# Kernel optimization log

Hardware: AMD Instinct MI355X
Metric: run time of the kernel (lower is better)

Reference implementation:

```python
import jax, jax.numpy as jnp
import numpy as np

D_K = 64  # key/query head dim used for the 1/sqrt(d_k) scale


def setup_inputs() -> dict:
    key0 = jax.random.key(0)
    kk, kq, kv = jax.random.split(key0, 3)
    B, H, S, DK, DV = 2, 16, 2048, 64, 64
    return {
        "key": jax.random.normal(kk, (B, H, S, DK), dtype=jnp.float32),
        "query": jax.random.normal(kq, (B, H, S, DK), dtype=jnp.float32),
        "value": jax.random.normal(kv, (B, H, S, DV), dtype=jnp.float32),
    }


def reference(key, query, value):
    # scaled dot-product attention per head: [B,H,S,S]
    scores = jnp.einsum("bhqd,bhkd->bhqk", query, key) / jnp.sqrt(jnp.asarray(D_K, query.dtype))
    attn = jax.nn.softmax(scores, axis=-1)
    out = jnp.einsum("bhqk,bhkv->bhqv", attn, value)  # [B,H,S,d_v]
    B, H, S, DV = out.shape
    # faithful to the torch .view: raw reshape (no head transpose)
    return out.reshape(B, S, H * DV)
```

## Files before the change

### kernel.cpp

```cpp
#include <hip/hip_runtime.h>

#define S_LEN 2048
#define DHEAD 64
#define BHEADS 32
#define NTILES 32
#define HEAD_ELEMS (S_LEN * DHEAD)
#define TENS_ELEMS (BHEADS * HEAD_ELEMS)
#define TILE_HALVES 4096

typedef _Float16 half8_t __attribute__((ext_vector_type(8)));
typedef _Float16 half4_t __attribute__((ext_vector_type(4)));
typedef _Float16 half2_t __attribute__((ext_vector_type(2)));
typedef float float4_t __attribute__((ext_vector_type(4)));

#define SC_LOG2E 0.18033688011112042f


__global__ __launch_bounds__(256) void prep_kernel(const float* __restrict__ K,
                                                   const float* __restrict__ V,
                                                   _Float16* __restrict__ Kf,
                                                   _Float16* __restrict__ Vf) {
    __shared__ _Float16 tile[64][72];
    const int bh = blockIdx.x >> 5;
    const int t = blockIdx.x & 31;
    const int tid = threadIdx.x;

    const float* Ksrc = K + (bh * S_LEN + t * 64) * DHEAD;
    const float4* vs = (const float4*)(V + (bh * S_LEN + t * 64) * DHEAD);
#pragma unroll
    for (int it = 0; it < 4; ++it) {
        int i = it * 256 + tid;
        float4 vv = vs[i];
        int r = i >> 4, c4 = (i & 15) * 4;
        half4_t hv = {(_Float16)vv.x, (_Float16)vv.y, (_Float16)vv.z, (_Float16)vv.w};
        *(half4_t*)&tile[r][c4] = hv;
    }

    _Float16* kd = Kf + (bh * NTILES + t) * TILE_HALVES;
#pragma unroll
    for (int it = 0; it < 2; ++it) {
        int c = it * 256 + tid;
        int f = c >> 6, lane = c & 63;
        int row = (f >> 1) * 16 + (lane & 15);
        int d0 = (f & 1) * 32 + (lane >> 4) * 8;
        const float4* s = (const float4*)(Ksrc + row * DHEAD + d0);
        float4 a = s[0], b = s[1];
        half8_t h = {(_Float16)(a.x * SC_LOG2E), (_Float16)(a.y * SC_LOG2E),
                     (_Float16)(a.z * SC_LOG2E), (_Float16)(a.w * SC_LOG2E),
                     (_Float16)(b.x * SC_LOG2E), (_Float16)(b.y * SC_LOG2E),
                     (_Float16)(b.z * SC_LOG2E), (_Float16)(b.w * SC_LOG2E)};
        *(half8_t*)(kd + c * 8) = h;
    }
    __syncthreads();

    _Float16* vd = Vf + (bh * NTILES + t) * TILE_HALVES;
#pragma unroll
    for (int it = 0; it < 2; ++it) {
        int c = it * 256 + tid;
        int fv = c >> 6, lane = c & 63;
        int vt = fv >> 1, ktp = fv & 1;
        int v = vt * 16 + (lane & 15);
        int g = lane >> 4;
        half8_t h;
#pragma unroll
        for (int j = 0; j < 8; ++j) {
            int key = ktp * 32 + (j >> 2) * 16 + g * 4 + (j & 3);
            h[j] = tile[key][v];
        }
        *(half8_t*)(vd + c * 8) = h;
    }
}


__global__ __launch_bounds__(256, 4) void attn_kernel(
    const float* __restrict__ Qf,
    const _Float16* __restrict__ Kf,
    const _Float16* __restrict__ Vf,
    float* __restrict__ out) {
    __shared__ float red[2][34][64];

    const int tid = threadIdx.x;
    const int wid = tid >> 6;
    const int lane = tid & 63;
    const int ln15 = lane & 15;
    const int g = lane >> 4;

    const int bh = blockIdx.x & 31;
    const int qidx = blockIdx.x >> 5;
    const int qsub = wid >> 1;
    const int ks = wid & 1;
    const int q0 = qidx * 64 + qsub * 32;
    const int t0 = ks * 16;

    const float* Qg = Qf + (bh * S_LEN + q0) * DHEAD;
    half8_t qf[2][2];
#pragma unroll
    for (int nq = 0; nq < 2; ++nq)
#pragma unroll
        for (int kh = 0; kh < 2; ++kh) {
            const float4* qs = (const float4*)(Qg + (nq * 16 + ln15) * DHEAD + kh * 32 + g * 8);
            float4 a = qs[0], b = qs[1];
            qf[nq][kh] = (half8_t){(_Float16)a.x, (_Float16)a.y, (_Float16)a.z, (_Float16)a.w,
                                   (_Float16)b.x, (_Float16)b.y, (_Float16)b.z, (_Float16)b.w};
        }

    const _Float16* kb = Kf + bh * (NTILES * TILE_HALVES) + t0 * TILE_HALVES;
    const _Float16* vb = Vf + bh * (NTILES * TILE_HALVES) + t0 * TILE_HALVES;
    const int lo = lane * 8;

    float lsum[2] = {0.f, 0.f};
    float4_t o[2][4];
#pragma unroll
    for (int nq = 0; nq < 2; ++nq)
#pragma unroll
        for (int vt = 0; vt < 4; ++vt) o[nq][vt] = (float4_t){0.f, 0.f, 0.f, 0.f};

#pragma unroll 2
    for (int t = 0; t < 16; ++t) {
        const int base = t * TILE_HALVES;

#pragma unroll
        for (int c = 0; c < 2; ++c) {
            half8_t kA[4], vA[4];
#pragma unroll
            for (int i = 0; i < 4; ++i)
                kA[i] = *(const half8_t*)(kb + base + (4 * c + i) * 512 + lo);
#pragma unroll
            for (int vt = 0; vt < 4; ++vt)
                vA[vt] = *(const half8_t*)(vb + base + (vt * 2 + c) * 512 + lo);

            half8_t pb[2];
#pragma unroll
            for (int h = 0; h < 2; ++h) {
                half8_t a0 = kA[h * 2];
                half8_t a1 = kA[h * 2 + 1];
#pragma unroll
                for (int nq = 0; nq < 2; ++nq) {
                    float4_t c0 = (float4_t){0.f, 0.f, 0.f, 0.f};
                    c0 = __builtin_amdgcn_mfma_f32_16x16x32_f16(a0, qf[nq][0], c0, 0, 0, 0);
                    c0 = __builtin_amdgcn_mfma_f32_16x16x32_f16(a1, qf[nq][1], c0, 0, 0, 0);
                    float p0 = __builtin_amdgcn_exp2f(c0[0]);
                    float p1 = __builtin_amdgcn_exp2f(c0[1]);
                    float p2 = __builtin_amdgcn_exp2f(c0[2]);
                    float p3 = __builtin_amdgcn_exp2f(c0[3]);
                    lsum[nq] += (p0 + p1) + (p2 + p3);
                    half2_t plo = __builtin_bit_cast(half2_t, __builtin_amdgcn_cvt_pkrtz(p0, p1));
                    half2_t phi = __builtin_bit_cast(half2_t, __builtin_amdgcn_cvt_pkrtz(p2, p3));
                    pb[nq][h * 4 + 0] = plo[0];
                    pb[nq][h * 4 + 1] = plo[1];
                    pb[nq][h * 4 + 2] = phi[0];
                    pb[nq][h * 4 + 3] = phi[1];
                }
            }
#pragma unroll
            for (int vt = 0; vt < 4; ++vt) {
                half8_t va = vA[vt];
#pragma unroll
                for (int nq = 0; nq < 2; ++nq)
                    o[nq][vt] = __builtin_amdgcn_mfma_f32_16x16x32_f16(va, pb[nq], o[nq][vt], 0, 0, 0);
            }
        }
    }

#pragma unroll
    for (int nq = 0; nq < 2; ++nq) {
        float l = lsum[nq];
        l += __shfl_xor(l, 16, 64);
        l += __shfl_xor(l, 32, 64);
        lsum[nq] = l;
    }

    if (ks == 1) {
#pragma unroll
        for (int nq = 0; nq < 2; ++nq)
#pragma unroll
            for (int vt = 0; vt < 4; ++vt)
#pragma unroll
                for (int r = 0; r < 4; ++r)
                    red[qsub][nq * 16 + vt * 4 + r][lane] = o[nq][vt][r];
#pragma unroll
        for (int nq = 0; nq < 2; ++nq) red[qsub][32 + nq][lane] = lsum[nq];
    }
    __syncthreads();
    if (ks == 0) {
#pragma unroll
        for (int nq = 0; nq < 2; ++nq) {
            float lt = lsum[nq] + red[qsub][32 + nq][lane];
            float inv_l = 1.0f / lt;
            int qg_global = q0 + nq * 16 + ln15;
            float* og = out + (bh * S_LEN + qg_global) * DHEAD;
#pragma unroll
            for (int vt = 0; vt < 4; ++vt) {
                float4_t vals;
#pragma unroll
                for (int r = 0; r < 4; ++r)
                    vals[r] = (o[nq][vt][r] + red[qsub][nq * 16 + vt * 4 + r][lane]) * inv_l;
                *(float4_t*)(og + vt * 16 + g * 4) = vals;
            }
        }
    }
}


extern "C" void kernel_launch(void* const* d_in, const int* in_sizes, int n_in,
                              void* d_out, int out_size, void* d_ws, size_t ws_size,
                              hipStream_t stream) {
    const float* Kin = (const float*)d_in[0];
    const float* Qin = (const float*)d_in[1];
    const float* Vin = (const float*)d_in[2];
    float* out = (float*)d_out;

    _Float16* Kf = (_Float16*)d_ws;
    _Float16* Vf = Kf + TENS_ELEMS;

    prep_kernel<<<BHEADS * NTILES, 256, 0, stream>>>(Kin, Vin, Kf, Vf);
    attn_kernel<<<BHEADS * 32, 256, 0, stream>>>(Qin, Kf, Vf, out);
}
```

Before: 133.5 us.

## Stage K/V tiles into LDS with double-buffered async loads, 512-thread blocks

The attention kernel now runs 512-thread blocks covering 128 queries, so four query-subgroups share each K/V tile. Tiles are staged into a 64KB LDS double buffer with global_load_lds, and each wave fetches a quarter of the chunks for the next tile while the current one is computed. This replaces per-wave direct global reads of K/V, with the aim of cutting redundant L2/global traffic and hiding load latency. In exchange it adds a block-wide barrier every iteration, and the large LDS footprint limits occupancy to about one block per CU. The reduction buffer aliases the K/V staging area.

```diff
diff --git a/kernel.cpp b/kernel.cpp
--- a/kernel.cpp
+++ b/kernel.cpp
@@ -15,6 +15,12 @@
 
 #define SC_LOG2E 0.18033688011112042f
 
+
+typedef const __attribute__((address_space(1))) unsigned int gas_u32;
+typedef __attribute__((address_space(3))) unsigned int las_u32;
+__device__ __forceinline__ void stage16(const void* g, void* l) {
+    __builtin_amdgcn_global_load_lds((gas_u32*)g, (las_u32*)l, 16, 0, 0);
+}
 
 __global__ __launch_bounds__(256) void prep_kernel(const float* __restrict__ K,
                                                    const float* __restrict__ V,
@@ -72,12 +78,14 @@
 }
 
 
-__global__ __launch_bounds__(256, 4) void attn_kernel(
+__global__ __launch_bounds__(512, 4) void attn_kernel(
     const float* __restrict__ Qf,
     const _Float16* __restrict__ Kf,
     const _Float16* __restrict__ Vf,
     float* __restrict__ out) {
-    __shared__ float red[2][34][64];
+    __shared__ __align__(16) char smem[65536];
+    _Float16 (*kv)[2][2][TILE_HALVES] = (_Float16 (*)[2][2][TILE_HALVES])smem;
+    float (*red)[34][64] = (float (*)[34][64])smem;
 
     const int tid = threadIdx.x;
     const int wid = tid >> 6;
@@ -89,7 +97,7 @@
     const int qidx = blockIdx.x >> 5;
     const int qsub = wid >> 1;
     const int ks = wid & 1;
-    const int q0 = qidx * 64 + qsub * 32;
+    const int q0 = qidx * 128 + qsub * 32;
     const int t0 = ks * 16;
 
     const float* Qg = Qf + (bh * S_LEN + q0) * DHEAD;
@@ -108,6 +116,8 @@
     const _Float16* vb = Vf + bh * (NTILES * TILE_HALVES) + t0 * TILE_HALVES;
     const int lo = lane * 8;
 
+    const int c0 = qsub * 4;
+
     float lsum[2] = {0.f, 0.f};
     float4_t o[2][4];
 #pragma unroll
@@ -115,19 +125,40 @@
 #pragma unroll
         for (int vt = 0; vt < 4; ++vt) o[nq][vt] = (float4_t){0.f, 0.f, 0.f, 0.f};
 
+#pragma unroll
+    for (int i = 0; i < 4; ++i) {
+        int c = c0 + i;
+        const _Float16* gs = (c < 8 ? kb : vb) + (c & 7) * 512 + lo;
+        stage16(gs, &kv[ks][0][c >> 3][(c & 7) * 512]);
+    }
+    __syncthreads();
+
 #pragma unroll 2
     for (int t = 0; t < 16; ++t) {
-        const int base = t * TILE_HALVES;
+        const int buf = t & 1;
+
+        if (t < 15) {
+            const int nb = (t + 1) * TILE_HALVES;
+#pragma unroll
+            for (int i = 0; i < 4; ++i) {
+                int c = c0 + i;
+                const _Float16* gs = (c < 8 ? kb : vb) + nb + (c & 7) * 512 + lo;
+                stage16(gs, &kv[ks][buf ^ 1][c >> 3][(c & 7) * 512]);
+            }
+        }
+
+        const _Float16* kl = &kv[ks][buf][0][0];
+        const _Float16* vl = &kv[ks][buf][1][0];
 
 #pragma unroll
         for (int c = 0; c < 2; ++c) {
             half8_t kA[4], vA[4];
 #pragma unroll
             for (int i = 0; i < 4; ++i)
-                kA[i] = *(const half8_t*)(kb + base + (4 * c + i) * 512 + lo);
+                kA[i] = *(const half8_t*)(kl + (4 * c + i) * 512 + lo);
 #pragma unroll
             for (int vt = 0; vt < 4; ++vt)
-                vA[vt] = *(const half8_t*)(vb + base + (vt * 2 + c) * 512 + lo);
+                vA[vt] = *(const half8_t*)(vl + (vt * 2 + c) * 512 + lo);
 
             half8_t pb[2];
 #pragma unroll
@@ -136,13 +167,13 @@
                 half8_t a1 = kA[h * 2 + 1];
 #pragma unroll
                 for (int nq = 0; nq < 2; ++nq) {
-                    float4_t c0 = (float4_t){0.f, 0.f, 0.f, 0.f};
-                    c0 = __builtin_amdgcn_mfma_f32_16x16x32_f16(a0, qf[nq][0], c0, 0, 0, 0);
-                    c0 = __builtin_amdgcn_mfma_f32_16x16x32_f16(a1, qf[nq][1], c0, 0, 0, 0);
-                    float p0 = __builtin_amdgcn_exp2f(c0[0]);
-                    float p1 = __builtin_amdgcn_exp2f(c0[1]);
-                    float p2 = __builtin_amdgcn_exp2f(c0[2]);
-                    float p3 = __builtin_amdgcn_exp2f(c0[3]);
+                    float4_t s0 = (float4_t){0.f, 0.f, 0.f, 0.f};
+                    s0 = __builtin_amdgcn_mfma_f32_16x16x32_f16(a0, qf[nq][0], s0, 0, 0, 0);
+                    s0 = __builtin_amdgcn_mfma_f32_16x16x32_f16(a1, qf[nq][1], s0, 0, 0, 0);
+                    float p0 = __builtin_amdgcn_exp2f(s0[0]);
+                    float p1 = __builtin_amdgcn_exp2f(s0[1]);
+                    float p2 = __builtin_amdgcn_exp2f(s0[2]);
+                    float p3 = __builtin_amdgcn_exp2f(s0[3]);
                     lsum[nq] += (p0 + p1) + (p2 + p3);
                     half2_t plo = __builtin_bit_cast(half2_t, __builtin_amdgcn_cvt_pkrtz(p0, p1));
                     half2_t phi = __builtin_bit_cast(half2_t, __builtin_amdgcn_cvt_pkrtz(p2, p3));
@@ -160,6 +191,8 @@
                     o[nq][vt] = __builtin_amdgcn_mfma_f32_16x16x32_f16(va, pb[nq], o[nq][vt], 0, 0, 0);
             }
         }
+
+        __syncthreads();
     }
 
 #pragma unroll
@@ -214,5 +247,5 @@
     _Float16* Vf = Kf + TENS_ELEMS;
 
     prep_kernel<<<BHEADS * NTILES, 256, 0, stream>>>(Kin, Vin, Kf, Vf);
-    attn_kernel<<<BHEADS * 32, 256, 0, stream>>>(Qin, Kf, Vf, out);
-}
+    attn_kernel<<<BHEADS * 16, 512, 0, stream>>>(Qin, Kf, Vf, out);
+}
```

New measurement: 130.3 us. -2.4%, faster.

## Warp-specialize attention into QK/exp producer and PV consumer waves via LDS

Applied to the files above, without the earlier changes.

Splits each block's waves into producer waves that compute QK^T scores and exp2 for 128 queries, and consumer waves that run the PV MFMAs. Probabilities pass through double-buffered LDS with a block barrier each step. Q is staged in LDS, each block now covers 128 queries so K/V are reused more and half as many blocks launch, and the occupancy hint drops to 2 blocks. The intent is to overlap the exp/transcendental work with the PV matrix work. The cost is 32 LDS barriers per block, extra LDS traffic, lower occupancy, and a large accumulator register footprint (8x4 float4 per consumer wave).

```diff
diff --git a/kernel.cpp b/kernel.cpp
--- a/kernel.cpp
+++ b/kernel.cpp
@@ -72,12 +72,15 @@
 }
 
 
-__global__ __launch_bounds__(256, 4) void attn_kernel(
+__global__ __launch_bounds__(256, 2) void attn_kernel(
     const float* __restrict__ Qf,
     const _Float16* __restrict__ Kf,
     const _Float16* __restrict__ Vf,
     float* __restrict__ out) {
-    __shared__ float red[2][34][64];
+    __shared__ __align__(16) char smem[49152];
+    _Float16* pbp = (_Float16*)smem;
+    _Float16* qls = (_Float16*)(smem + 32768);
+    float (*red)[64] = (float (*)[64])smem;
 
     const int tid = threadIdx.x;
     const int wid = tid >> 6;
@@ -87,114 +90,148 @@
 
     const int bh = blockIdx.x & 31;
     const int qidx = blockIdx.x >> 5;
-    const int qsub = wid >> 1;
-    const int ks = wid & 1;
-    const int q0 = qidx * 64 + qsub * 32;
-    const int t0 = ks * 16;
-
-    const float* Qg = Qf + (bh * S_LEN + q0) * DHEAD;
-    half8_t qf[2][2];
-#pragma unroll
-    for (int nq = 0; nq < 2; ++nq)
-#pragma unroll
-        for (int kh = 0; kh < 2; ++kh) {
+    const int ks = wid >> 1;
+    const int role = (wid ^ (int)blockIdx.x) & 1;
+    const int q0 = qidx * 128;
+    const int lo = lane * 8;
+
+    {
+        const float* Qg = Qf + (bh * S_LEN + q0) * DHEAD;
+#pragma unroll
+        for (int i = 0; i < 4; ++i) {
+            int nq = wid * 2 + (i >> 1);
+            int kh = i & 1;
             const float4* qs = (const float4*)(Qg + (nq * 16 + ln15) * DHEAD + kh * 32 + g * 8);
             float4 a = qs[0], b = qs[1];
-            qf[nq][kh] = (half8_t){(_Float16)a.x, (_Float16)a.y, (_Float16)a.z, (_Float16)a.w,
-                                   (_Float16)b.x, (_Float16)b.y, (_Float16)b.z, (_Float16)b.w};
-        }
-
-    const _Float16* kb = Kf + bh * (NTILES * TILE_HALVES) + t0 * TILE_HALVES;
-    const _Float16* vb = Vf + bh * (NTILES * TILE_HALVES) + t0 * TILE_HALVES;
-    const int lo = lane * 8;
-
-    float lsum[2] = {0.f, 0.f};
-    float4_t o[2][4];
-#pragma unroll
-    for (int nq = 0; nq < 2; ++nq)
+            half8_t h = {(_Float16)a.x, (_Float16)a.y, (_Float16)a.z, (_Float16)a.w,
+                         (_Float16)b.x, (_Float16)b.y, (_Float16)b.z, (_Float16)b.w};
+            *(half8_t*)(qls + (nq * 2 + kh) * 512 + lo) = h;
+        }
+    }
+    __syncthreads();
+
+    const _Float16* kb = Kf + bh * (NTILES * TILE_HALVES) + ks * 16 * TILE_HALVES;
+    const _Float16* vb = Vf + bh * (NTILES * TILE_HALVES) + ks * 16 * TILE_HALVES;
+
+    float4_t o[8][4];
+    float lsum[8];
+#pragma unroll
+    for (int nq = 0; nq < 8; ++nq) {
+        lsum[nq] = 0.f;
 #pragma unroll
         for (int vt = 0; vt < 4; ++vt) o[nq][vt] = (float4_t){0.f, 0.f, 0.f, 0.f};
+    }
 
 #pragma unroll 2
-    for (int t = 0; t < 16; ++t) {
-        const int base = t * TILE_HALVES;
-
-#pragma unroll
-        for (int c = 0; c < 2; ++c) {
-            half8_t kA[4], vA[4];
+    for (int p = 0; p < 32; ++p) {
+        if (role == 0) {
+            const int t = p >> 1, c = p & 1;
+            const int base = t * TILE_HALVES;
+            half8_t kA[4];
 #pragma unroll
             for (int i = 0; i < 4; ++i)
                 kA[i] = *(const half8_t*)(kb + base + (4 * c + i) * 512 + lo);
+            _Float16* pbw = pbp + (ks * 2 + (p & 1)) * 4096 + lo;
+#pragma unroll
+            for (int nq = 0; nq < 8; ++nq) {
+                half8_t q0f = *(const half8_t*)(qls + (nq * 2 + 0) * 512 + lo);
+                half8_t q1f = *(const half8_t*)(qls + (nq * 2 + 1) * 512 + lo);
+                float4_t a0 = (float4_t){0.f, 0.f, 0.f, 0.f};
+                float4_t a1 = (float4_t){0.f, 0.f, 0.f, 0.f};
+                a0 = __builtin_amdgcn_mfma_f32_16x16x32_f16(kA[0], q0f, a0, 0, 0, 0);
+                a0 = __builtin_amdgcn_mfma_f32_16x16x32_f16(kA[1], q1f, a0, 0, 0, 0);
+                a1 = __builtin_amdgcn_mfma_f32_16x16x32_f16(kA[2], q0f, a1, 0, 0, 0);
+                a1 = __builtin_amdgcn_mfma_f32_16x16x32_f16(kA[3], q1f, a1, 0, 0, 0);
+                float p0 = __builtin_amdgcn_exp2f(a0[0]);
+                float p1 = __builtin_amdgcn_exp2f(a0[1]);
+                float p2 = __builtin_amdgcn_exp2f(a0[2]);
+                float p3 = __builtin_amdgcn_exp2f(a0[3]);
+                float p4 = __builtin_amdgcn_exp2f(a1[0]);
+                float p5 = __builtin_amdgcn_exp2f(a1[1]);
+                float p6 = __builtin_amdgcn_exp2f(a1[2]);
+                float p7 = __builtin_amdgcn_exp2f(a1[3]);
+                half2_t e01 = __builtin_bit_cast(half2_t, __builtin_amdgcn_cvt_pkrtz(p0, p1));
+                half2_t e23 = __builtin_bit_cast(half2_t, __builtin_amdgcn_cvt_pkrtz(p2, p3));
+                half2_t e45 = __builtin_bit_cast(half2_t, __builtin_amdgcn_cvt_pkrtz(p4, p5));
+                half2_t e67 = __builtin_bit_cast(half2_t, __builtin_amdgcn_cvt_pkrtz(p6, p7));
+                half8_t pbreg = {e01[0], e01[1], e23[0], e23[1],
+                                 e45[0], e45[1], e67[0], e67[1]};
+                *(half8_t*)(pbw + nq * 512) = pbreg;
+            }
+        } else if (p > 0) {
+            const int tc = p - 1;
+            const int t = tc >> 1, c = tc & 1, rbuf = tc & 1;
+            const int base = t * TILE_HALVES;
+            half8_t vA[4];
 #pragma unroll
             for (int vt = 0; vt < 4; ++vt)
                 vA[vt] = *(const half8_t*)(vb + base + (vt * 2 + c) * 512 + lo);
-
-            half8_t pb[2];
-#pragma unroll
-            for (int h = 0; h < 2; ++h) {
-                half8_t a0 = kA[h * 2];
-                half8_t a1 = kA[h * 2 + 1];
-#pragma unroll
-                for (int nq = 0; nq < 2; ++nq) {
-                    float4_t c0 = (float4_t){0.f, 0.f, 0.f, 0.f};
-                    c0 = __builtin_amdgcn_mfma_f32_16x16x32_f16(a0, qf[nq][0], c0, 0, 0, 0);
-                    c0 = __builtin_amdgcn_mfma_f32_16x16x32_f16(a1, qf[nq][1], c0, 0, 0, 0);
-                    float p0 = __builtin_amdgcn_exp2f(c0[0]);
-                    float p1 = __builtin_amdgcn_exp2f(c0[1]);
-                    float p2 = __builtin_amdgcn_exp2f(c0[2]);
-                    float p3 = __builtin_amdgcn_exp2f(c0[3]);
-                    lsum[nq] += (p0 + p1) + (p2 + p3);
-                    half2_t plo = __builtin_bit_cast(half2_t, __builtin_amdgcn_cvt_pkrtz(p0, p1));
-                    half2_t phi = __builtin_bit_cast(half2_t, __builtin_amdgcn_cvt_pkrtz(p2, p3));
-                    pb[nq][h * 4 + 0] = plo[0];
-                    pb[nq][h * 4 + 1] = plo[1];
-                    pb[nq][h * 4 + 2] = phi[0];
-                    pb[nq][h * 4 + 3] = phi[1];
-                }
+            const _Float16* pbr0 = pbp + (ks * 2 + rbuf) * 4096 + lo;
+#pragma unroll
+            for (int nq = 0; nq < 8; ++nq) {
+                half8_t pbr = *(const half8_t*)(pbr0 + nq * 512);
+#pragma unroll
+                for (int vt = 0; vt < 4; ++vt)
+                    o[nq][vt] = __builtin_amdgcn_mfma_f32_16x16x32_f16(vA[vt], pbr, o[nq][vt], 0, 0, 0);
+                lsum[nq] += ((float)pbr[0] + (float)pbr[1]) + ((float)pbr[2] + (float)pbr[3])
+                          + ((float)pbr[4] + (float)pbr[5]) + ((float)pbr[6] + (float)pbr[7]);
             }
-#pragma unroll
-            for (int vt = 0; vt < 4; ++vt) {
-                half8_t va = vA[vt];
-#pragma unroll
-                for (int nq = 0; nq < 2; ++nq)
-                    o[nq][vt] = __builtin_amdgcn_mfma_f32_16x16x32_f16(va, pb[nq], o[nq][vt], 0, 0, 0);
-            }
-        }
-    }
-
-#pragma unroll
-    for (int nq = 0; nq < 2; ++nq) {
-        float l = lsum[nq];
-        l += __shfl_xor(l, 16, 64);
-        l += __shfl_xor(l, 32, 64);
-        lsum[nq] = l;
-    }
-
-    if (ks == 1) {
-#pragma unroll
-        for (int nq = 0; nq < 2; ++nq)
+        }
+        __syncthreads();
+    }
+
+    if (role == 1) {
+        const int t = 15, c = 1, rbuf = 1;
+        const int base = t * TILE_HALVES;
+        half8_t vA[4];
+#pragma unroll
+        for (int vt = 0; vt < 4; ++vt)
+            vA[vt] = *(const half8_t*)(vb + base + (vt * 2 + c) * 512 + lo);
+        const _Float16* pbr0 = pbp + (ks * 2 + rbuf) * 4096 + lo;
+#pragma unroll
+        for (int nq = 0; nq < 8; ++nq) {
+            half8_t pbr = *(const half8_t*)(pbr0 + nq * 512);
 #pragma unroll
             for (int vt = 0; vt < 4; ++vt)
+                o[nq][vt] = __builtin_amdgcn_mfma_f32_16x16x32_f16(vA[vt], pbr, o[nq][vt], 0, 0, 0);
+            lsum[nq] += ((float)pbr[0] + (float)pbr[1]) + ((float)pbr[2] + (float)pbr[3])
+                      + ((float)pbr[4] + (float)pbr[5]) + ((float)pbr[6] + (float)pbr[7]);
+        }
+#pragma unroll
+        for (int nq = 0; nq < 8; ++nq) {
+            float l = lsum[nq];
+            l += __shfl_xor(l, 16, 64);
+            l += __shfl_xor(l, 32, 64);
+            lsum[nq] = l;
+        }
+    }
+    __syncthreads();
+
+    if (role == 1 && ks == 1) {
+#pragma unroll
+        for (int nq = 0; nq < 8; ++nq) {
+#pragma unroll
+            for (int vt = 0; vt < 4; ++vt)
 #pragma unroll
                 for (int r = 0; r < 4; ++r)
-                    red[qsub][nq * 16 + vt * 4 + r][lane] = o[nq][vt][r];
-#pragma unroll
-        for (int nq = 0; nq < 2; ++nq) red[qsub][32 + nq][lane] = lsum[nq];
-    }
-    __syncthreads();
-    if (ks == 0) {
-#pragma unroll
-        for (int nq = 0; nq < 2; ++nq) {
-            float lt = lsum[nq] + red[qsub][32 + nq][lane];
+                    red[nq * 16 + vt * 4 + r][lane] = o[nq][vt][r];
+            red[128 + nq][lane] = lsum[nq];
+        }
+    }
+    __syncthreads();
+    if (role == 1 && ks == 0) {
+#pragma unroll
+        for (int nq = 0; nq < 8; ++nq) {
+            float lt = lsum[nq] + red[128 + nq][lane];
             float inv_l = 1.0f / lt;
-            int qg_global = q0 + nq * 16 + ln15;
-            float* og = out + (bh * S_LEN + qg_global) * DHEAD;
+            int qrow = q0 + nq * 16 + ln15;
+            float* og = out + (bh * S_LEN + qrow) * DHEAD;
 #pragma unroll
             for (int vt = 0; vt < 4; ++vt) {
                 float4_t vals;
 #pragma unroll
                 for (int r = 0; r < 4; ++r)
-                    vals[r] = (o[nq][vt][r] + red[qsub][nq * 16 + vt * 4 + r][lane]) * inv_l;
+                    vals[r] = (o[nq][vt][r] + red[nq * 16 + vt * 4 + r][lane]) * inv_l;
                 *(float4_t*)(og + vt * 16 + g * 4) = vals;
             }
         }
@@ -214,5 +251,5 @@
     _Float16* Vf = Kf + TENS_ELEMS;
 
     prep_kernel<<<BHEADS * NTILES, 256, 0, stream>>>(Kin, Vin, Kf, Vf);
-    attn_kernel<<<BHEADS * 32, 256, 0, stream>>>(Qin, Kf, Vf, out);
+    attn_kernel<<<BHEADS * 16, 256, 0, stream>>>(Qin, Kf, Vf, out);
 }
```

New measurement: 132.5 us. About the same (-0.8%).
